# Kernel optimization log

Hardware: AMD Instinct MI355X
Metric: run time of the kernel (lower is better)

## Reference

```python
import jax, jax.numpy as jnp
import numpy as np

B = 16384          # batch_size
NL = 4096          # nb_labels
T = 64             # max_num_trials


def setup_inputs() -> dict:
    key = jax.random.key(0)
    k1, k2 = jax.random.split(key)
    inputs = jax.random.normal(k1, (B, NL), dtype=jnp.float32)
    # targets are one-hot (original code takes argmax to find the single positive)
    labels = jax.random.randint(k2, (B,), 0, NL)
    targets = jax.nn.one_hot(labels, NL, dtype=jnp.float32)
    return {"inputs": inputs, "targets": targets}


def _warp_forward(inputs, targets, max_num_trials=T, sample_key=jax.random.key(42)):
    # Sequential uniform sampling WITHOUT replacement from the remaining negative
    # set == walking a uniform random permutation of the negatives. We realize the
    # permutation with iid uniform noise + argsort, then find the first trial whose
    # margin is > 0 (the while-loop exit condition).
    bsz, nb_labels = inputs.shape
    pos_idx = jnp.argmax(targets, axis=1)                                  # [B]
    pos_score = jnp.take_along_axis(inputs, pos_idx[:, None], axis=1)      # [B,1]

    noise = jax.random.uniform(sample_key, (bsz, nb_labels))               # [B,NL]
    # force the positive label to sort last so the first NL-1 slots are negatives
    noise = noise.at[jnp.arange(bsz), pos_idx].set(-1.0)
    order = jnp.argsort(-noise, axis=1)[:, :max_num_trials]                # [B,T] random negative order

    neg_scores = jnp.take_along_axis(inputs, order, axis=1)                # [B,T]
    margins = 1.0 + neg_scores - pos_score                                 # [B,T]

    hit = margins > 0.0
    found = jnp.any(hit, axis=1)                                           # [B]
    first = jnp.argmax(hit, axis=1)                                        # first trial with margin>0
    num_trials = jnp.where(found, first + 1, max_num_trials)               # [B]
    pick_col = jnp.where(found, first, max_num_trials - 1)
    neg_idx = jnp.take_along_axis(order, pick_col[:, None], axis=1)[:, 0]  # [B]
    # original: after the loop, set loss unless final margin < 0
    set_flag = found | (margins[:, -1] >= 0.0)                             # [B]

    loss_weight = jnp.log(jnp.floor((nb_labels - 1.0) / num_trials.astype(jnp.float32)))
    L = jnp.where(set_flag, loss_weight, 0.0)                              # [B]

    neg_onehot = jnp.zeros_like(inputs).at[jnp.arange(bsz), neg_idx].add(
        set_flag.astype(inputs.dtype))                                     # [B,NL]

    loss = L * (1.0 - jnp.sum(targets * inputs, axis=1)
                + jnp.sum(neg_onehot * inputs, axis=1))                    # [B]
    return jnp.sum(loss, axis=0, keepdims=True)                            # [1]


def reference(inputs, targets):
    return _warp_forward(inputs, targets)
```

## Files before the change

### kernel.cpp

```cpp
#include <hip/hip_runtime.h>
#include <stdint.h>

#define NLBL      4096
#define HALF_ROWS 8192
#define HALF_CNT  33554432u
#define TPB       512

__device__ __forceinline__ uint32_t rotl32(uint32_t x, uint32_t r) {
    return (x << r) | (x >> (32u - r));
}

__device__ __forceinline__ void threefry2x32(uint32_t x0, uint32_t x1,
                                             uint32_t& o0, uint32_t& o1) {
    const uint32_t ks0 = 0u;
    const uint32_t ks1 = 42u;
    const uint32_t ks2 = 0x1BD11BDAu ^ ks0 ^ ks1;
    x0 += ks0; x1 += ks1;
#define TF_RND(r) x0 += x1; x1 = rotl32(x1, (r)); x1 ^= x0;
    TF_RND(13u) TF_RND(15u) TF_RND(26u) TF_RND(6u)
    x0 += ks1; x1 += ks2 + 1u;
    TF_RND(17u) TF_RND(29u) TF_RND(16u) TF_RND(24u)
    x0 += ks2; x1 += ks0 + 2u;
    TF_RND(13u) TF_RND(15u) TF_RND(26u) TF_RND(6u)
    x0 += ks0; x1 += ks1 + 3u;
    TF_RND(17u) TF_RND(29u) TF_RND(16u) TF_RND(24u)
    x0 += ks1; x1 += ks2 + 4u;
    TF_RND(13u) TF_RND(15u) TF_RND(26u) TF_RND(6u)
    x0 += ks2; x1 += ks0 + 5u;
#undef TF_RND
    o0 = x0; o1 = x1;
}


__global__ void __launch_bounds__(TPB)
warp_loss_main(const float* __restrict__ inputs,
               const float* __restrict__ targets,
               float* __restrict__ out)
{
    const int b   = blockIdx.x;
    const int tid = threadIdx.x;
    const size_t r0 = (size_t)b * NLBL;
    const size_t r1 = (size_t)(b + HALF_ROWS) * NLBL;

    const float4* in0 = reinterpret_cast<const float4*>(inputs  + r0);
    const float4* in1 = reinterpret_cast<const float4*>(inputs  + r1);
    const float4* tg0 = reinterpret_cast<const float4*>(targets + r0);
    const float4* tg1 = reinterpret_cast<const float4*>(targets + r1);

    __shared__ float              s_sc[2][NLBL];
    __shared__ int                s_pos[2];
    __shared__ float              s_psc[2];
    __shared__ unsigned long long s_key[2][8];
    __shared__ unsigned int       s_cnt[8];
    __shared__ int                s_cstar[2];
    __shared__ uint32_t           s_nb[2];

    uint32_t ub0[8], ub1[8];
    const uint32_t cbase0 = (uint32_t)b * NLBL;

    #pragma unroll
    for (int kc = 0; kc < 2; ++kc) {
        const int v4 = tid + (kc << 9);
        const int c  = v4 << 2;

        const float4 a0 = in0[v4];
        const float4 a1 = in1[v4];
        const float4 t0 = tg0[v4];
        const float4 t1 = tg1[v4];

        #pragma unroll
        for (int j = 0; j < 4; ++j) {
            const uint32_t i = cbase0 + (uint32_t)(c + j);
            uint32_t o0, o1;
            threefry2x32(i, i + HALF_CNT, o0, o1);
            ub0[kc*4+j] = o0 >> 9;
            ub1[kc*4+j] = o1 >> 9;
        }

        reinterpret_cast<float4*>(s_sc[0])[v4] = a0;
        reinterpret_cast<float4*>(s_sc[1])[v4] = a1;

        if (t0.x > 0.5f) { s_pos[0] = c + 0; s_psc[0] = a0.x; }
        if (t0.y > 0.5f) { s_pos[0] = c + 1; s_psc[0] = a0.y; }
        if (t0.z > 0.5f) { s_pos[0] = c + 2; s_psc[0] = a0.z; }
        if (t0.w > 0.5f) { s_pos[0] = c + 3; s_psc[0] = a0.w; }
        if (t1.x > 0.5f) { s_pos[1] = c + 0; s_psc[1] = a1.x; }
        if (t1.y > 0.5f) { s_pos[1] = c + 1; s_psc[1] = a1.y; }
        if (t1.z > 0.5f) { s_pos[1] = c + 2; s_psc[1] = a1.z; }
        if (t1.w > 0.5f) { s_pos[1] = c + 3; s_psc[1] = a1.w; }
    }
    __syncthreads();

    const int   pos0 = s_pos[0], pos1 = s_pos[1];
    const float psc0 = s_psc[0], psc1 = s_psc[1];

    unsigned long long key0 = 0ull, key1 = 0ull;
    #pragma unroll
    for (int kc = 0; kc < 2; ++kc) {
        const int v4 = tid + (kc << 9);
        const float4 x0 = reinterpret_cast<const float4*>(s_sc[0])[v4];
        const float4 x1 = reinterpret_cast<const float4*>(s_sc[1])[v4];
        const float q0[4] = { x0.x, x0.y, x0.z, x0.w };
        const float q1[4] = { x1.x, x1.y, x1.z, x1.w };
        #pragma unroll
        for (int j = 0; j < 4; ++j) {
            const int c = (v4 << 2) + j;
            const int k = kc*4 + j;
            const float m0 = (1.0f + q0[j]) - psc0;
            const float m1 = (1.0f + q1[j]) - psc1;
            if (c != pos0 && m0 > 0.0f) {
                const unsigned long long kk =
                    ((unsigned long long)(ub0[k] + 1u) << 12) | (unsigned long long)(4095 - c);
                if (kk > key0) key0 = kk;
            }
            if (c != pos1 && m1 > 0.0f) {
                const unsigned long long kk =
                    ((unsigned long long)(ub1[k] + 1u) << 12) | (unsigned long long)(4095 - c);
                if (kk > key1) key1 = kk;
            }
        }
    }
    #pragma unroll
    for (int off = 32; off; off >>= 1) {
        const unsigned long long q0 = __shfl_xor(key0, off);
        const unsigned long long q1 = __shfl_xor(key1, off);
        if (q0 > key0) key0 = q0;
        if (q1 > key1) key1 = q1;
    }
    const int wv = tid >> 6;
    if ((tid & 63) == 0) { s_key[0][wv] = key0; s_key[1][wv] = key1; }
    __syncthreads();
    if (tid == 0) {
        #pragma unroll
        for (int r = 0; r < 2; ++r) {
            unsigned long long kk = s_key[r][0];
            #pragma unroll
            for (int w = 1; w < 8; ++w) if (s_key[r][w] > kk) kk = s_key[r][w];
            if (kk == 0ull) {
                s_cstar[r] = -1;
                s_nb[r]    = 0xFFFFFFFFu;
            } else {
                s_cstar[r] = 4095 - (int)(kk & 0xFFFull);
                s_nb[r]    = (uint32_t)(kk >> 12) - 1u;
            }
        }
    }
    __syncthreads();

    const int      c0  = s_cstar[0], c1  = s_cstar[1];
    const uint32_t nb0 = s_nb[0],    nb1 = s_nb[1];

    uint32_t cnt = 0;
    #pragma unroll
    for (int k = 0; k < 8; ++k) {
        const int c = (tid << 2) + ((k >> 2) << 11) + (k & 3);
        if (c0 >= 0 && c != pos0 && (ub0[k] > nb0 || (ub0[k] == nb0 && c < c0))) cnt += 1u;
        if (c1 >= 0 && c != pos1 && (ub1[k] > nb1 || (ub1[k] == nb1 && c < c1))) cnt += 1u << 16;
    }
    #pragma unroll
    for (int off = 32; off; off >>= 1) cnt += __shfl_xor(cnt, off);
    if ((tid & 63) == 0) s_cnt[wv] = cnt;
    __syncthreads();

    if (tid == 0) {
        uint32_t tot = 0;
        #pragma unroll
        for (int w = 0; w < 8; ++w) tot += s_cnt[w];
        const int rank0 = (int)(tot & 0xFFFFu);
        const int rank1 = (int)(tot >> 16);
        float total = 0.0f;
        if (c0 >= 0 && rank0 < 64) {
            const float margin = (1.0f - psc0) + s_sc[0][c0];
            total += logf(floorf(4095.0f / (float)(rank0 + 1))) * margin;
        }
        if (c1 >= 0 && rank1 < 64) {
            const float margin = (1.0f - psc1) + s_sc[1][c1];
            total += logf(floorf(4095.0f / (float)(rank1 + 1))) * margin;
        }
        if (total != 0.0f) atomicAdd(out, total);
    }
}

extern "C" void kernel_launch(void* const* d_in, const int* in_sizes, int n_in,
                              void* d_out, int out_size, void* d_ws, size_t ws_size,
                              hipStream_t stream) {
    const float* inputs  = (const float*)d_in[0];
    const float* targets = (const float*)d_in[1];
    float* out = (float*)d_out;

    hipMemsetAsync(out, 0, sizeof(float), stream);
    warp_loss_main<<<dim3(HALF_ROWS), dim3(TPB), 0, stream>>>(inputs, targets, out);
}
```

Before: 526.1 us.

## Hoist all loads before RNG, drop serial sync stage, replace atomics with reduce kernel

All eight float4 global loads are issued up front, before the threefry RNG work, so memory latency can overlap with the integer hashing. The rotate is expressed as a single alignbit instruction. The per-block key reduction is now done redundantly by every thread, which removes one __syncthreads and a tid==0 serial section, and the positive score is read from shared memory instead of being stored separately. The global atomicAdd and the memset are replaced by per-block partial sums written to the workspace and summed by a second single-block kernel, at the cost of an extra launch.

```diff
diff --git a/kernel.cpp b/kernel.cpp
--- a/kernel.cpp
+++ b/kernel.cpp
@@ -7,7 +7,7 @@
 #define TPB       512
 
 __device__ __forceinline__ uint32_t rotl32(uint32_t x, uint32_t r) {
-    return (x << r) | (x >> (32u - r));
+    return __builtin_amdgcn_alignbit(x, x, 32u - r);
 }
 
 __device__ __forceinline__ void threefry2x32(uint32_t x0, uint32_t x1,
@@ -35,7 +35,7 @@
 __global__ void __launch_bounds__(TPB)
 warp_loss_main(const float* __restrict__ inputs,
                const float* __restrict__ targets,
-               float* __restrict__ out)
+               float* __restrict__ part)
 {
     const int b   = blockIdx.x;
     const int tid = threadIdx.x;
@@ -49,25 +49,26 @@
 
     __shared__ float              s_sc[2][NLBL];
     __shared__ int                s_pos[2];
-    __shared__ float              s_psc[2];
     __shared__ unsigned long long s_key[2][8];
     __shared__ unsigned int       s_cnt[8];
-    __shared__ int                s_cstar[2];
-    __shared__ uint32_t           s_nb[2];
 
     uint32_t ub0[8], ub1[8];
     const uint32_t cbase0 = (uint32_t)b * NLBL;
 
+    const int v4a = tid;
+    const int v4b = tid + 512;
+    const float4 a0A = in0[v4a];
+    const float4 a0B = in0[v4b];
+    const float4 a1A = in1[v4a];
+    const float4 a1B = in1[v4b];
+    const float4 t0A = tg0[v4a];
+    const float4 t0B = tg0[v4b];
+    const float4 t1A = tg1[v4a];
+    const float4 t1B = tg1[v4b];
+
     #pragma unroll
     for (int kc = 0; kc < 2; ++kc) {
-        const int v4 = tid + (kc << 9);
-        const int c  = v4 << 2;
-
-        const float4 a0 = in0[v4];
-        const float4 a1 = in1[v4];
-        const float4 t0 = tg0[v4];
-        const float4 t1 = tg1[v4];
-
+        const int c = (tid + (kc << 9)) << 2;
         #pragma unroll
         for (int j = 0; j < 4; ++j) {
             const uint32_t i = cbase0 + (uint32_t)(c + j);
@@ -76,23 +77,29 @@
             ub0[kc*4+j] = o0 >> 9;
             ub1[kc*4+j] = o1 >> 9;
         }
-
-        reinterpret_cast<float4*>(s_sc[0])[v4] = a0;
-        reinterpret_cast<float4*>(s_sc[1])[v4] = a1;
-
-        if (t0.x > 0.5f) { s_pos[0] = c + 0; s_psc[0] = a0.x; }
-        if (t0.y > 0.5f) { s_pos[0] = c + 1; s_psc[0] = a0.y; }
-        if (t0.z > 0.5f) { s_pos[0] = c + 2; s_psc[0] = a0.z; }
-        if (t0.w > 0.5f) { s_pos[0] = c + 3; s_psc[0] = a0.w; }
-        if (t1.x > 0.5f) { s_pos[1] = c + 0; s_psc[1] = a1.x; }
-        if (t1.y > 0.5f) { s_pos[1] = c + 1; s_psc[1] = a1.y; }
-        if (t1.z > 0.5f) { s_pos[1] = c + 2; s_psc[1] = a1.z; }
-        if (t1.w > 0.5f) { s_pos[1] = c + 3; s_psc[1] = a1.w; }
-    }
-    __syncthreads();
-
-    const int   pos0 = s_pos[0], pos1 = s_pos[1];
-    const float psc0 = s_psc[0], psc1 = s_psc[1];
+    }
+
+    reinterpret_cast<float4*>(s_sc[0])[v4a] = a0A;
+    reinterpret_cast<float4*>(s_sc[0])[v4b] = a0B;
+    reinterpret_cast<float4*>(s_sc[1])[v4a] = a1A;
+    reinterpret_cast<float4*>(s_sc[1])[v4b] = a1B;
+
+    {
+        const int cA = v4a << 2, cB = v4b << 2;
+        if (t0A.x > 0.5f || t0A.y > 0.5f || t0A.z > 0.5f || t0A.w > 0.5f)
+            s_pos[0] = cA + (t0A.x > 0.5f ? 0 : (t0A.y > 0.5f ? 1 : (t0A.z > 0.5f ? 2 : 3)));
+        if (t0B.x > 0.5f || t0B.y > 0.5f || t0B.z > 0.5f || t0B.w > 0.5f)
+            s_pos[0] = cB + (t0B.x > 0.5f ? 0 : (t0B.y > 0.5f ? 1 : (t0B.z > 0.5f ? 2 : 3)));
+        if (t1A.x > 0.5f || t1A.y > 0.5f || t1A.z > 0.5f || t1A.w > 0.5f)
+            s_pos[1] = cA + (t1A.x > 0.5f ? 0 : (t1A.y > 0.5f ? 1 : (t1A.z > 0.5f ? 2 : 3)));
+        if (t1B.x > 0.5f || t1B.y > 0.5f || t1B.z > 0.5f || t1B.w > 0.5f)
+            s_pos[1] = cB + (t1B.x > 0.5f ? 0 : (t1B.y > 0.5f ? 1 : (t1B.z > 0.5f ? 2 : 3)));
+    }
+    __syncthreads();
+
+    const int   pos0 = s_pos[0],       pos1 = s_pos[1];
+    const float psc0 = s_sc[0][pos0];
+    const float psc1 = s_sc[1][pos1];
 
     unsigned long long key0 = 0ull, key1 = 0ull;
     #pragma unroll
@@ -130,25 +137,17 @@
     const int wv = tid >> 6;
     if ((tid & 63) == 0) { s_key[0][wv] = key0; s_key[1][wv] = key1; }
     __syncthreads();
-    if (tid == 0) {
-        #pragma unroll
-        for (int r = 0; r < 2; ++r) {
-            unsigned long long kk = s_key[r][0];
-            #pragma unroll
-            for (int w = 1; w < 8; ++w) if (s_key[r][w] > kk) kk = s_key[r][w];
-            if (kk == 0ull) {
-                s_cstar[r] = -1;
-                s_nb[r]    = 0xFFFFFFFFu;
-            } else {
-                s_cstar[r] = 4095 - (int)(kk & 0xFFFull);
-                s_nb[r]    = (uint32_t)(kk >> 12) - 1u;
-            }
-        }
-    }
-    __syncthreads();
-
-    const int      c0  = s_cstar[0], c1  = s_cstar[1];
-    const uint32_t nb0 = s_nb[0],    nb1 = s_nb[1];
+
+    unsigned long long kk0 = s_key[0][0], kk1 = s_key[1][0];
+    #pragma unroll
+    for (int w = 1; w < 8; ++w) {
+        if (s_key[0][w] > kk0) kk0 = s_key[0][w];
+        if (s_key[1][w] > kk1) kk1 = s_key[1][w];
+    }
+    const int      c0  = (kk0 == 0ull) ? -1 : 4095 - (int)(kk0 & 0xFFFull);
+    const int      c1  = (kk1 == 0ull) ? -1 : 4095 - (int)(kk1 & 0xFFFull);
+    const uint32_t nb0 = (kk0 == 0ull) ? 0xFFFFFFFFu : (uint32_t)(kk0 >> 12) - 1u;
+    const uint32_t nb1 = (kk1 == 0ull) ? 0xFFFFFFFFu : (uint32_t)(kk1 >> 12) - 1u;
 
     uint32_t cnt = 0;
     #pragma unroll
@@ -177,7 +176,27 @@
             const float margin = (1.0f - psc1) + s_sc[1][c1];
             total += logf(floorf(4095.0f / (float)(rank1 + 1))) * margin;
         }
-        if (total != 0.0f) atomicAdd(out, total);
+        part[b] = total;
+    }
+}
+
+__global__ void __launch_bounds__(1024)
+warp_loss_reduce(const float* __restrict__ part, float* __restrict__ out)
+{
+    const int tid = threadIdx.x;
+    const float4 a = reinterpret_cast<const float4*>(part)[tid];
+    const float4 b = reinterpret_cast<const float4*>(part)[tid + 1024];
+    float s = ((a.x + a.y) + (a.z + a.w)) + ((b.x + b.y) + (b.z + b.w));
+    #pragma unroll
+    for (int off = 32; off; off >>= 1) s += __shfl_xor(s, off);
+    __shared__ float sm[16];
+    if ((tid & 63) == 0) sm[tid >> 6] = s;
+    __syncthreads();
+    if (tid == 0) {
+        float t = 0.0f;
+        #pragma unroll
+        for (int w = 0; w < 16; ++w) t += sm[w];
+        out[0] = t;
     }
 }
 
@@ -186,8 +205,9 @@
                               hipStream_t stream) {
     const float* inputs  = (const float*)d_in[0];
     const float* targets = (const float*)d_in[1];
-    float* out = (float*)d_out;
-
-    hipMemsetAsync(out, 0, sizeof(float), stream);
-    warp_loss_main<<<dim3(HALF_ROWS), dim3(TPB), 0, stream>>>(inputs, targets, out);
-}
+    float* out  = (float*)d_out;
+    float* part = (float*)d_ws;
+
+    warp_loss_main  <<<dim3(HALF_ROWS), dim3(TPB),  0, stream>>>(inputs, targets, part);
+    warp_loss_reduce<<<dim3(1),         dim3(1024), 0, stream>>>(part, out);
+}
```

After: 520.2 us. Within noise of the previous version (-1.1%).
